# Kernel optimization log

Measured on AMD Instinct MI355X. Metric: run time of the kernel, lower is better.

Reference implementation:

```python
import jax, jax.numpy as jnp
import numpy as np

B, N, D, E, H = 4, 1024, 1024, 8, 4096


def setup_inputs() -> dict:
    key = jax.random.key(0)
    ks = jax.random.split(key, 8)
    x = jax.random.normal(ks[0], (B, N, D), dtype=jnp.float32)
    # gumbel noise, matching F.gumbel_softmax's -log(-log(U))
    u = jax.random.uniform(ks[1], (B * N, E), dtype=jnp.float32, minval=1e-9, maxval=1.0)
    gumbel = -jnp.log(-jnp.log(u))
    router_w = jax.random.normal(ks[2], (D, E), dtype=jnp.float32) * 0.02
    router_b = jnp.zeros((E,), dtype=jnp.float32)
    w1 = jax.random.normal(ks[3], (E, D, H), dtype=jnp.float32) * 0.02
    b1 = jnp.zeros((E, H), dtype=jnp.float32)
    w2 = jax.random.normal(ks[4], (E, H, D), dtype=jnp.float32) * 0.02
    b2 = jnp.zeros((E, D), dtype=jnp.float32)
    return {"x": x, "gumbel": gumbel, "router_w": router_w, "router_b": router_b,
            "w1": w1, "b1": b1, "w2": w2, "b2": b2}


def reference(x, gumbel, router_w, router_b, w1, b1, w2, b2):
    b, n, d = x.shape
    e = router_w.shape[1]
    xf = x.reshape(-1, d)                      # (T, D), T = B*N tokens
    logits = xf @ router_w + router_b          # (T, E)

    # hard gumbel-softmax with straight-through estimator (tau = 1.0)
    y_soft = jax.nn.softmax(logits + gumbel, axis=-1)
    hard = jax.nn.one_hot(jnp.argmax(y_soft, axis=-1), e, dtype=y_soft.dtype)
    weights = hard - jax.lax.stop_gradient(y_soft) + y_soft   # (T, E)

    # load-balancing aux loss
    probs = jax.nn.softmax(logits, axis=-1)
    count = jnp.maximum(jnp.float32(xf.shape[0]), 1.0)
    importance = probs.sum(axis=0) / count
    aux_loss = jnp.mean((importance - 1.0 / e) ** 2)

    # dense all-expert FFN: every expert processes every token
    hidden = jax.nn.gelu(jnp.einsum('td,edh->eth', xf, w1) + b1[:, None, :],
                         approximate=False)                    # (E, T, H)
    expert_out = jnp.einsum('eth,ehd->etd', hidden, w2) + b2[:, None, :]  # (E, T, D)

    # weighted combine (einsum 'ej,ejd->jd' in the original)
    out = jnp.einsum('te,etd->td', weights, expert_out)        # (T, D)
    return out.reshape(b, n, d), aux_loss
```

## Files before the change

kernel.cpp:

```cpp
#include <hip/hip_runtime.h>
#include <math.h>

#define D_DIM 1024
#define MAX_TILES 40

typedef __attribute__((ext_vector_type(4))) float f32x4;
typedef __attribute__((ext_vector_type(8))) short s16x8;

__device__ __forceinline__ unsigned short f2bf(float f){
  union { float f; unsigned u; } v; v.f = f;
  unsigned r = v.u + 0x7FFFu + ((v.u >> 16) & 1u);
  return (unsigned short)(r >> 16);
}

__device__ __forceinline__ void gld_lds16(const unsigned short* g, unsigned short* l){
  __builtin_amdgcn_global_load_lds(
      (const __attribute__((address_space(1))) unsigned int*)g,
      (__attribute__((address_space(3))) unsigned int*)l, 16, 0, 0);
}

template<int N>
__device__ __forceinline__ void wait_vmcnt(){
  if constexpr (N == 8)      asm volatile("s_waitcnt vmcnt(8)" ::: "memory");
  else if constexpr (N == 6) asm volatile("s_waitcnt vmcnt(6)" ::: "memory");
  else                       asm volatile("s_waitcnt vmcnt(0)" ::: "memory");
  __builtin_amdgcn_sched_barrier(0);
}

__global__ __launch_bounds__(256) void router_kernel(
    const float* __restrict__ x, const float* __restrict__ gumbel,
    const float* __restrict__ rw, const float* __restrict__ rb,
    int* __restrict__ expert_id, float* __restrict__ wtok,
    double* __restrict__ prob_sums, int* __restrict__ counts)
{
  int wave = threadIdx.x >> 6, lane = threadIdx.x & 63;
  int t = blockIdx.x * 4 + wave;
  const float* xr = x + (size_t)t * D_DIM;
  double acc[8];
  #pragma unroll
  for (int e = 0; e < 8; e++) acc[e] = 0.0;
  #pragma unroll
  for (int i = 0; i < 16; i++){
    int d = i * 64 + lane;
    double xv = (double)xr[d];
    const float4* rwp = (const float4*)(rw + (size_t)d * 8);
    float4 r0 = rwp[0], r1 = rwp[1];
    acc[0] += xv * (double)r0.x; acc[1] += xv * (double)r0.y;
    acc[2] += xv * (double)r0.z; acc[3] += xv * (double)r0.w;
    acc[4] += xv * (double)r1.x; acc[5] += xv * (double)r1.y;
    acc[6] += xv * (double)r1.z; acc[7] += xv * (double)r1.w;
  }
  #pragma unroll
  for (int e = 0; e < 8; e++){
    #pragma unroll
    for (int off = 32; off; off >>= 1) acc[e] += __shfl_xor(acc[e], off);
  }
  double logit[8], z[8];
  #pragma unroll
  for (int e = 0; e < 8; e++){
    logit[e] = acc[e] + (double)rb[e];
    z[e] = logit[e] + (double)gumbel[(size_t)t * 8 + e];
  }
  int amax = 0;
  #pragma unroll
  for (int e = 1; e < 8; e++) if (z[e] > z[amax]) amax = e;
  float zm = (float)z[amax];
  float se = 0.f;
  #pragma unroll
  for (int e = 0; e < 8; e++) se += expf((float)z[e] - zm);
  float y = 1.f / se;
  float w = (1.0f - y) + y;
  double lm = logit[0];
  #pragma unroll
  for (int e = 1; e < 8; e++) lm = fmax(lm, logit[e]);
  float p[8]; float ps = 0.f;
  #pragma unroll
  for (int e = 0; e < 8; e++){ p[e] = expf((float)(logit[e] - lm)); ps += p[e]; }
  float inv = 1.f / ps;

  __shared__ float sprob[4][8];
  if (lane == 0){
    expert_id[t] = amax; wtok[t] = w;
    atomicAdd(&counts[amax], 1);
    #pragma unroll
    for (int e = 0; e < 8; e++) sprob[wave][e] = p[e] * inv;
  }
  __syncthreads();
  if (threadIdx.x < 8){
    double s = (double)sprob[0][threadIdx.x] + (double)sprob[1][threadIdx.x]
             + (double)sprob[2][threadIdx.x] + (double)sprob[3][threadIdx.x];
    atomicAdd(&prob_sums[threadIdx.x], s);
  }
}

__global__ void finalize_kernel(const double* __restrict__ prob_sums, const int* __restrict__ counts,
                                int* __restrict__ offsets, int* __restrict__ cursor,
                                int* __restrict__ tile_e, int* __restrict__ tile_start,
                                int* __restrict__ tile_rows, int* __restrict__ n_mtiles,
                                float* __restrict__ aux_out)
{
  if (threadIdx.x == 0){
    int off = 0, m = 0;
    for (int e = 0; e < 8; e++){
      offsets[e] = off; cursor[e] = off;
      int c = counts[e];
      for (int by = 0; by * 128 < c; by++){
        tile_e[m] = e;
        tile_start[m] = off + by * 128;
        int r = c - by * 128;
        tile_rows[m] = r < 128 ? r : 128;
        m++;
      }
      off += c;
    }
    n_mtiles[0] = m;
    double aux = 0.0;
    for (int e = 0; e < 8; e++){
      double d = prob_sums[e] / 4096.0 - 0.125;
      aux += d * d;
    }
    aux_out[0] = (float)(aux / 8.0);
  }
}

__global__ __launch_bounds__(256) void scatter_kernel(
    const float* __restrict__ x, const int* __restrict__ expert_id, const float* __restrict__ wtok,
    int* __restrict__ cursor, int* __restrict__ token_of, float* __restrict__ gw,
    unsigned short* __restrict__ Xg)
{
  int t = blockIdx.x;
  __shared__ int spos;
  if (threadIdx.x == 0){
    int e = expert_id[t];
    int p = atomicAdd(&cursor[e], 1);
    spos = p;
    token_of[p] = t; gw[p] = wtok[t];
  }
  __syncthreads();
  int pos = spos;
  float4 v = ((const float4*)(x + (size_t)t * D_DIM))[threadIdx.x];
  ushort4 o; o.x = f2bf(v.x); o.y = f2bf(v.y); o.z = f2bf(v.z); o.w = f2bf(v.w);
  ((ushort4*)(Xg + (size_t)pos * D_DIM))[threadIdx.x] = o;
}

__global__ __launch_bounds__(256) void transpose_w(
    const float* __restrict__ W, unsigned short* __restrict__ WT, int K, int N)
{
  int e = blockIdx.z;
  int k0 = blockIdx.x * 64;
  int n0 = blockIdx.y * 64;
  __shared__ float tile[64][65];
  const float* src = W + (size_t)e * K * N;
  int tid = threadIdx.x;
  int r = tid >> 4;
  int c4 = (tid & 15) * 4;
  #pragma unroll
  for (int j = 0; j < 4; j++){
    int k = r + j * 16;
    float4 v = *(const float4*)(src + (size_t)(k0 + k) * N + n0 + c4);
    tile[k][c4] = v.x; tile[k][c4 + 1] = v.y; tile[k][c4 + 2] = v.z; tile[k][c4 + 3] = v.w;
  }
  __syncthreads();
  unsigned short* dst = WT + (size_t)e * N * K;
  #pragma unroll
  for (int it = 0; it < 2; it++){
    int idx = it * 256 + tid;
    int n = idx >> 3;
    int s = idx & 7;
    unsigned short buf[8];
    #pragma unroll
    for (int j = 0; j < 8; j++) buf[j] = f2bf(tile[s * 8 + j][n]);
    *(s16x8*)(dst + (size_t)(n0 + n) * K + k0 + s * 8) = *(s16x8*)buf;
  }
}

template<int K, int N, int BN, int PASS2>
__global__ __launch_bounds__(256, 2) void ffn_gemm(
    const unsigned short* __restrict__ A,
    const unsigned short* __restrict__ BT,
    const float* __restrict__ bias,
    const int* __restrict__ tile_e, const int* __restrict__ tile_start,
    const int* __restrict__ tile_rows, const int* __restrict__ n_mtiles,
    const int* __restrict__ token_of, const float* __restrict__ gw,
    unsigned short* __restrict__ Hout,
    float* __restrict__ Fout)
{
  int mt = blockIdx.y;
  if (mt >= n_mtiles[0]) return;
  int e = tile_e[mt], tstart = tile_start[mt], trows = tile_rows[mt];
  int bx = blockIdx.x;
  int tid = threadIdx.x, lane = tid & 63;
  int wv = __builtin_amdgcn_readfirstlane(tid >> 6);
  int wm = wv & 1, wn = wv >> 1;
  constexpr int NI    = BN / 32;
  constexpr int NBW   = BN / 32;
  constexpr int NK    = K / 64;
  constexpr int LOADS = 4 + NBW;

  __shared__ unsigned short sA[2][128 * 64];
  __shared__ unsigned short sB[2][BN * 64];

  int r8  = lane >> 3;
  int swz = ((lane & 7) ^ r8) * 8;

  const unsigned short* ap[4]; int al[4];
  #pragma unroll
  for (int j = 0; j < 4; j++){
    int c = wv * 4 + j;
    int row = c * 8 + r8;
    int rr = row < trows ? row : 0;
    ap[j] = A + (size_t)(tstart + rr) * K + swz;
    al[j] = c * 512;
  }
  const unsigned short* bp[NBW]; int bl[NBW];
  #pragma unroll
  for (int j = 0; j < NBW; j++){
    int c = wv * NBW + j;
    int n = bx * BN + c * 8 + r8;
    bp[j] = BT + ((size_t)e * N + n) * K + swz;
    bl[j] = c * 512;
  }

  f32x4 accv[4][NI];
  #pragma unroll
  for (int mi = 0; mi < 4; mi++)
    #pragma unroll
    for (int ni = 0; ni < NI; ni++) accv[mi][ni] = (f32x4){0.f, 0.f, 0.f, 0.f};

  #pragma unroll
  for (int b = 0; b < 2; b++){
    #pragma unroll
    for (int j = 0; j < 4; j++){ gld_lds16(ap[j], &sA[b][al[j]]); ap[j] += 64; }
    #pragma unroll
    for (int j = 0; j < NBW; j++){ gld_lds16(bp[j], &sB[b][bl[j]]); bp[j] += 64; }
  }

  int col = lane & 15, quad = lane >> 4, rx = col & 7;
  for (int kt = 0; kt < NK; ++kt){
    int cur = kt & 1;
    if (kt + 1 < NK) wait_vmcnt<LOADS>(); else wait_vmcnt<0>();
    __builtin_amdgcn_s_barrier();
    s16x8 af[2][4], bfr[2][NI];
    #pragma unroll
    for (int kh = 0; kh < 2; kh++){
      int ps = ((kh * 4 + quad) ^ rx) * 8;
      #pragma unroll
      for (int mi = 0; mi < 4; mi++)
        af[kh][mi] = *(const s16x8*)&sA[cur][(wm * 64 + mi * 16 + col) * 64 + ps];
      #pragma unroll
      for (int ni = 0; ni < NI; ni++)
        bfr[kh][ni] = *(const s16x8*)&sB[cur][(wn * (BN / 2) + ni * 16 + col) * 64 + ps];
    }
    asm volatile("s_waitcnt lgkmcnt(0)" ::: "memory");
    __builtin_amdgcn_sched_barrier(0);
    __builtin_amdgcn_s_barrier();
    if (kt + 2 < NK){
      #pragma unroll
      for (int j = 0; j < 4; j++){ gld_lds16(ap[j], &sA[cur][al[j]]); ap[j] += 64; }
      #pragma unroll
      for (int j = 0; j < NBW; j++){ gld_lds16(bp[j], &sB[cur][bl[j]]); bp[j] += 64; }
    }
    __builtin_amdgcn_s_setprio(1);
    #pragma unroll
    for (int kh = 0; kh < 2; kh++)
      #pragma unroll
      for (int mi = 0; mi < 4; mi++)
        #pragma unroll
        for (int ni = 0; ni < NI; ni++)
          accv[mi][ni] = __builtin_amdgcn_mfma_f32_16x16x32_bf16(af[kh][mi], bfr[kh][ni], accv[mi][ni], 0, 0, 0);
    __builtin_amdgcn_s_setprio(0);
  }

  float bv[NI];
  #pragma unroll
  for (int ni = 0; ni < NI; ni++)
    bv[ni] = bias[(size_t)e * N + bx * BN + wn * (BN / 2) + ni * 16 + col];

  if (PASS2 == 0){
    #pragma unroll
    for (int mi = 0; mi < 4; mi++){
      int rbase = wm * 64 + mi * 16 + quad * 4;
      #pragma unroll
      for (int r = 0; r < 4; r++){
        int row = rbase + r;
        if (row < trows){
          size_t orow = (size_t)(tstart + row) * N + bx * BN + wn * (BN / 2) + col;
          #pragma unroll
          for (int ni = 0; ni < NI; ni++){
            float v = accv[mi][ni][r] + bv[ni];
            float g = 0.5f * v * (1.0f + erff(v * 0.70710678118654752f));
            Hout[orow + ni * 16] = f2bf(g);
          }
        }
      }
    }
  } else {
    #pragma unroll
    for (int mi = 0; mi < 4; mi++){
      int rbase = wm * 64 + mi * 16 + quad * 4;
      #pragma unroll
      for (int r = 0; r < 4; r++){
        int row = rbase + r;
        if (row < trows){
          int pos = tstart + row;
          int tok = token_of[pos];
          float wgt = gw[pos];
          size_t orow = (size_t)tok * N + bx * BN + wn * (BN / 2) + col;
          #pragma unroll
          for (int ni = 0; ni < NI; ni++)
            Fout[orow + ni * 16] = (accv[mi][ni][r] + bv[ni]) * wgt;
        }
      }
    }
  }
}

extern "C" void kernel_launch(void* const* d_in, const int* in_sizes, int n_in,
                              void* d_out, int out_size, void* d_ws, size_t ws_size,
                              hipStream_t stream)
{
  const float* x      = (const float*)d_in[0];
  const float* gumbel = (const float*)d_in[1];
  const float* rw     = (const float*)d_in[2];
  const float* rb     = (const float*)d_in[3];
  const float* w1     = (const float*)d_in[4];
  const float* b1     = (const float*)d_in[5];
  const float* w2     = (const float*)d_in[6];
  const float* b2     = (const float*)d_in[7];
  float* out = (float*)d_out;

  char* ws = (char*)d_ws;
  double* prob_sums = (double*)(ws + 0);
  int* counts     = (int*)(ws + 64);
  int* offsets    = (int*)(ws + 96);
  int* cursor     = (int*)(ws + 128);
  int* n_mtiles   = (int*)(ws + 160);
  int* tile_e     = (int*)(ws + 192);
  int* tile_start = (int*)(ws + 384);
  int* tile_rows  = (int*)(ws + 576);
  int* expert_id  = (int*)(ws + 1024);
  float* wtok     = (float*)(ws + 1024 + 16384);
  int* token_of   = (int*)(ws + 1024 + 2 * 16384);
  float* gw       = (float*)(ws + 1024 + 3 * 16384);
  unsigned short* Xg     = (unsigned short*)(ws + 66560);
  unsigned short* hidden = (unsigned short*)(ws + 66560 + 8388608);
  unsigned short* wT     = (unsigned short*)(ws + 66560 + 8388608 + 33554432);

  hipMemsetAsync(ws, 0, 256, stream);

  router_kernel<<<1024, 256, 0, stream>>>(x, gumbel, rw, rb, expert_id, wtok, prob_sums, counts);
  finalize_kernel<<<1, 64, 0, stream>>>(prob_sums, counts, offsets, cursor,
                                        tile_e, tile_start, tile_rows, n_mtiles, out + 4194304);
  scatter_kernel<<<4096, 256, 0, stream>>>(x, expert_id, wtok, cursor, token_of, gw, Xg);

  transpose_w<<<dim3(16, 64, 8), 256, 0, stream>>>(w1, wT, 1024, 4096);
  ffn_gemm<1024, 4096, 128, 0><<<dim3(32, MAX_TILES), 256, 0, stream>>>(
      Xg, wT, b1, tile_e, tile_start, tile_rows, n_mtiles, nullptr, nullptr, hidden, nullptr);

  transpose_w<<<dim3(64, 16, 8), 256, 0, stream>>>(w2, wT, 4096, 1024);
  ffn_gemm<4096, 1024, 64, 1><<<dim3(16, MAX_TILES), 256, 0, stream>>>(
      hidden, wT, b2, tile_e, tile_start, tile_rows, n_mtiles, token_of, gw, nullptr, out);
}
```

Before: 544.8 us.

## Fuse weight transposes with router and scatter, widen second GEMM tile

Merges the w1 transpose with the router kernel and the w2 transpose with the token scatter kernel, so each pair runs as one launch with heterogeneous blocks. The two transposed weights now get separate workspace buffers, which allows the merge. The GEMM is fixed at a 128-wide N tile for both passes, so the second GEMM uses half as many blocks. Its k-loop is also restructured to issue the MFMAs for the first k-half while the second half's LDS reads are still in flight. This removes launch gaps and some serialization, at the cost of more workspace and less parallelism in the second GEMM.

```diff
diff --git a/kernel.cpp b/kernel.cpp
--- a/kernel.cpp
+++ b/kernel.cpp
@@ -19,22 +19,15 @@
       (__attribute__((address_space(3))) unsigned int*)l, 16, 0, 0);
 }
 
-template<int N>
-__device__ __forceinline__ void wait_vmcnt(){
-  if constexpr (N == 8)      asm volatile("s_waitcnt vmcnt(8)" ::: "memory");
-  else if constexpr (N == 6) asm volatile("s_waitcnt vmcnt(6)" ::: "memory");
-  else                       asm volatile("s_waitcnt vmcnt(0)" ::: "memory");
-  __builtin_amdgcn_sched_barrier(0);
-}
-
-__global__ __launch_bounds__(256) void router_kernel(
+__device__ __forceinline__ void router_body(
     const float* __restrict__ x, const float* __restrict__ gumbel,
     const float* __restrict__ rw, const float* __restrict__ rb,
     int* __restrict__ expert_id, float* __restrict__ wtok,
-    double* __restrict__ prob_sums, int* __restrict__ counts)
+    double* __restrict__ prob_sums, int* __restrict__ counts,
+    int rb_idx, float* sprob )
 {
   int wave = threadIdx.x >> 6, lane = threadIdx.x & 63;
-  int t = blockIdx.x * 4 + wave;
+  int t = rb_idx * 4 + wave;
   const float* xr = x + (size_t)t * D_DIM;
   double acc[8];
   #pragma unroll
@@ -78,18 +71,64 @@
   for (int e = 0; e < 8; e++){ p[e] = expf((float)(logit[e] - lm)); ps += p[e]; }
   float inv = 1.f / ps;
 
-  __shared__ float sprob[4][8];
   if (lane == 0){
     expert_id[t] = amax; wtok[t] = w;
     atomicAdd(&counts[amax], 1);
     #pragma unroll
-    for (int e = 0; e < 8; e++) sprob[wave][e] = p[e] * inv;
+    for (int e = 0; e < 8; e++) sprob[wave * 8 + e] = p[e] * inv;
   }
   __syncthreads();
   if (threadIdx.x < 8){
-    double s = (double)sprob[0][threadIdx.x] + (double)sprob[1][threadIdx.x]
-             + (double)sprob[2][threadIdx.x] + (double)sprob[3][threadIdx.x];
+    double s = (double)sprob[0 * 8 + threadIdx.x] + (double)sprob[1 * 8 + threadIdx.x]
+             + (double)sprob[2 * 8 + threadIdx.x] + (double)sprob[3 * 8 + threadIdx.x];
     atomicAdd(&prob_sums[threadIdx.x], s);
+  }
+}
+
+__device__ __forceinline__ void transpose_body(
+    const float* __restrict__ W, unsigned short* __restrict__ WT,
+    int K, int N, int kx, int ny, int e, float* tile )
+{
+  int k0 = kx * 64;
+  int n0 = ny * 64;
+  const float* src = W + (size_t)e * K * N;
+  int tid = threadIdx.x;
+  int r = tid >> 4;
+  int c4 = (tid & 15) * 4;
+  #pragma unroll
+  for (int j = 0; j < 4; j++){
+    int k = r + j * 16;
+    float4 v = *(const float4*)(src + (size_t)(k0 + k) * N + n0 + c4);
+    tile[k * 65 + c4] = v.x; tile[k * 65 + c4 + 1] = v.y;
+    tile[k * 65 + c4 + 2] = v.z; tile[k * 65 + c4 + 3] = v.w;
+  }
+  __syncthreads();
+  unsigned short* dst = WT + (size_t)e * N * K;
+  #pragma unroll
+  for (int it = 0; it < 2; it++){
+    int idx = it * 256 + tid;
+    int n = idx >> 3;
+    int s = idx & 7;
+    unsigned short buf[8];
+    #pragma unroll
+    for (int j = 0; j < 8; j++) buf[j] = f2bf(tile[(s * 8 + j) * 65 + n]);
+    *(s16x8*)(dst + (size_t)(n0 + n) * K + k0 + s * 8) = *(s16x8*)buf;
+  }
+}
+
+__global__ __launch_bounds__(256) void stage_a(
+    const float* __restrict__ w1, unsigned short* __restrict__ wT1,
+    const float* __restrict__ x, const float* __restrict__ gumbel,
+    const float* __restrict__ rw, const float* __restrict__ rb,
+    int* __restrict__ expert_id, float* __restrict__ wtok,
+    double* __restrict__ prob_sums, int* __restrict__ counts)
+{
+  __shared__ float smem[64 * 65];
+  int b = blockIdx.x;
+  if (b < 8192){
+    transpose_body(w1, wT1, 1024, 4096, b & 15, (b >> 4) & 63, b >> 10, smem);
+  } else {
+    router_body(x, gumbel, rw, rb, expert_id, wtok, prob_sums, counts, b - 8192, smem);
   }
 }
 
@@ -123,58 +162,35 @@
   }
 }
 
-__global__ __launch_bounds__(256) void scatter_kernel(
-    const float* __restrict__ x, const int* __restrict__ expert_id, const float* __restrict__ wtok,
-    int* __restrict__ cursor, int* __restrict__ token_of, float* __restrict__ gw,
+__global__ __launch_bounds__(256) void stage_b(
+    const float* __restrict__ w2, unsigned short* __restrict__ wT2,
+    const float* __restrict__ x, const int* __restrict__ expert_id,
+    const float* __restrict__ wtok, int* __restrict__ cursor,
+    int* __restrict__ token_of, float* __restrict__ gw,
     unsigned short* __restrict__ Xg)
 {
-  int t = blockIdx.x;
-  __shared__ int spos;
-  if (threadIdx.x == 0){
-    int e = expert_id[t];
-    int p = atomicAdd(&cursor[e], 1);
-    spos = p;
-    token_of[p] = t; gw[p] = wtok[t];
-  }
-  __syncthreads();
-  int pos = spos;
-  float4 v = ((const float4*)(x + (size_t)t * D_DIM))[threadIdx.x];
-  ushort4 o; o.x = f2bf(v.x); o.y = f2bf(v.y); o.z = f2bf(v.z); o.w = f2bf(v.w);
-  ((ushort4*)(Xg + (size_t)pos * D_DIM))[threadIdx.x] = o;
-}
-
-__global__ __launch_bounds__(256) void transpose_w(
-    const float* __restrict__ W, unsigned short* __restrict__ WT, int K, int N)
-{
-  int e = blockIdx.z;
-  int k0 = blockIdx.x * 64;
-  int n0 = blockIdx.y * 64;
-  __shared__ float tile[64][65];
-  const float* src = W + (size_t)e * K * N;
-  int tid = threadIdx.x;
-  int r = tid >> 4;
-  int c4 = (tid & 15) * 4;
-  #pragma unroll
-  for (int j = 0; j < 4; j++){
-    int k = r + j * 16;
-    float4 v = *(const float4*)(src + (size_t)(k0 + k) * N + n0 + c4);
-    tile[k][c4] = v.x; tile[k][c4 + 1] = v.y; tile[k][c4 + 2] = v.z; tile[k][c4 + 3] = v.w;
-  }
-  __syncthreads();
-  unsigned short* dst = WT + (size_t)e * N * K;
-  #pragma unroll
-  for (int it = 0; it < 2; it++){
-    int idx = it * 256 + tid;
-    int n = idx >> 3;
-    int s = idx & 7;
-    unsigned short buf[8];
-    #pragma unroll
-    for (int j = 0; j < 8; j++) buf[j] = f2bf(tile[s * 8 + j][n]);
-    *(s16x8*)(dst + (size_t)(n0 + n) * K + k0 + s * 8) = *(s16x8*)buf;
-  }
-}
-
-template<int K, int N, int BN, int PASS2>
+  __shared__ float smem[64 * 65];
+  int b = blockIdx.x;
+  if (b < 8192){
+    transpose_body(w2, wT2, 4096, 1024, b & 63, (b >> 6) & 15, b >> 10, smem);
+  } else {
+    int t = b - 8192;
+    int* spos = (int*)smem;
+    if (threadIdx.x == 0){
+      int e = expert_id[t];
+      int p = atomicAdd(&cursor[e], 1);
+      spos[0] = p;
+      token_of[p] = t; gw[p] = wtok[t];
+    }
+    __syncthreads();
+    int pos = spos[0];
+    float4 v = ((const float4*)(x + (size_t)t * D_DIM))[threadIdx.x];
+    ushort4 o; o.x = f2bf(v.x); o.y = f2bf(v.y); o.z = f2bf(v.z); o.w = f2bf(v.w);
+    ((ushort4*)(Xg + (size_t)pos * D_DIM))[threadIdx.x] = o;
+  }
+}
+
+template<int K, int N, int PASS2>
 __global__ __launch_bounds__(256, 2) void ffn_gemm(
     const unsigned short* __restrict__ A,
     const unsigned short* __restrict__ BT,
@@ -192,13 +208,10 @@
   int tid = threadIdx.x, lane = tid & 63;
   int wv = __builtin_amdgcn_readfirstlane(tid >> 6);
   int wm = wv & 1, wn = wv >> 1;
-  constexpr int NI    = BN / 32;
-  constexpr int NBW   = BN / 32;
-  constexpr int NK    = K / 64;
-  constexpr int LOADS = 4 + NBW;
+  constexpr int NK = K / 64;
 
   __shared__ unsigned short sA[2][128 * 64];
-  __shared__ unsigned short sB[2][BN * 64];
+  __shared__ unsigned short sB[2][128 * 64];
 
   int r8  = lane >> 3;
   int swz = ((lane & 7) ^ r8) * 8;
@@ -212,45 +225,60 @@
     ap[j] = A + (size_t)(tstart + rr) * K + swz;
     al[j] = c * 512;
   }
-  const unsigned short* bp[NBW]; int bl[NBW];
-  #pragma unroll
-  for (int j = 0; j < NBW; j++){
-    int c = wv * NBW + j;
-    int n = bx * BN + c * 8 + r8;
+  const unsigned short* bp[4]; int bl[4];
+  #pragma unroll
+  for (int j = 0; j < 4; j++){
+    int c = wv * 4 + j;
+    int n = bx * 128 + c * 8 + r8;
     bp[j] = BT + ((size_t)e * N + n) * K + swz;
     bl[j] = c * 512;
   }
 
-  f32x4 accv[4][NI];
+  f32x4 accv[4][4];
   #pragma unroll
   for (int mi = 0; mi < 4; mi++)
     #pragma unroll
-    for (int ni = 0; ni < NI; ni++) accv[mi][ni] = (f32x4){0.f, 0.f, 0.f, 0.f};
+    for (int ni = 0; ni < 4; ni++) accv[mi][ni] = (f32x4){0.f, 0.f, 0.f, 0.f};
 
   #pragma unroll
   for (int b = 0; b < 2; b++){
     #pragma unroll
     for (int j = 0; j < 4; j++){ gld_lds16(ap[j], &sA[b][al[j]]); ap[j] += 64; }
     #pragma unroll
-    for (int j = 0; j < NBW; j++){ gld_lds16(bp[j], &sB[b][bl[j]]); bp[j] += 64; }
+    for (int j = 0; j < 4; j++){ gld_lds16(bp[j], &sB[b][bl[j]]); bp[j] += 64; }
   }
 
   int col = lane & 15, quad = lane >> 4, rx = col & 7;
+  int ps0 = (quad ^ rx) * 8;
+  int ps1 = ((4 + quad) ^ rx) * 8;
   for (int kt = 0; kt < NK; ++kt){
     int cur = kt & 1;
-    if (kt + 1 < NK) wait_vmcnt<LOADS>(); else wait_vmcnt<0>();
+    if (kt + 1 < NK) asm volatile("s_waitcnt vmcnt(8)" ::: "memory");
+    else             asm volatile("s_waitcnt vmcnt(0)" ::: "memory");
+    __builtin_amdgcn_sched_barrier(0);
     __builtin_amdgcn_s_barrier();
-    s16x8 af[2][4], bfr[2][NI];
-    #pragma unroll
-    for (int kh = 0; kh < 2; kh++){
-      int ps = ((kh * 4 + quad) ^ rx) * 8;
-      #pragma unroll
-      for (int mi = 0; mi < 4; mi++)
-        af[kh][mi] = *(const s16x8*)&sA[cur][(wm * 64 + mi * 16 + col) * 64 + ps];
-      #pragma unroll
-      for (int ni = 0; ni < NI; ni++)
-        bfr[kh][ni] = *(const s16x8*)&sB[cur][(wn * (BN / 2) + ni * 16 + col) * 64 + ps];
-    }
+    s16x8 af0[4], bf0[4], af1[4], bf1[4];
+    #pragma unroll
+    for (int mi = 0; mi < 4; mi++)
+      af0[mi] = *(const s16x8*)&sA[cur][(wm * 64 + mi * 16 + col) * 64 + ps0];
+    #pragma unroll
+    for (int ni = 0; ni < 4; ni++)
+      bf0[ni] = *(const s16x8*)&sB[cur][(wn * 64 + ni * 16 + col) * 64 + ps0];
+    #pragma unroll
+    for (int mi = 0; mi < 4; mi++)
+      af1[mi] = *(const s16x8*)&sA[cur][(wm * 64 + mi * 16 + col) * 64 + ps1];
+    #pragma unroll
+    for (int ni = 0; ni < 4; ni++)
+      bf1[ni] = *(const s16x8*)&sB[cur][(wn * 64 + ni * 16 + col) * 64 + ps1];
+    asm volatile("s_waitcnt lgkmcnt(8)" ::: "memory");
+    __builtin_amdgcn_sched_barrier(0);
+    __builtin_amdgcn_s_setprio(1);
+    #pragma unroll
+    for (int mi = 0; mi < 4; mi++)
+      #pragma unroll
+      for (int ni = 0; ni < 4; ni++)
+        accv[mi][ni] = __builtin_amdgcn_mfma_f32_16x16x32_bf16(af0[mi], bf0[ni], accv[mi][ni], 0, 0, 0);
+    __builtin_amdgcn_s_setprio(0);
     asm volatile("s_waitcnt lgkmcnt(0)" ::: "memory");
     __builtin_amdgcn_sched_barrier(0);
     __builtin_amdgcn_s_barrier();
@@ -258,23 +286,21 @@
       #pragma unroll
       for (int j = 0; j < 4; j++){ gld_lds16(ap[j], &sA[cur][al[j]]); ap[j] += 64; }
       #pragma unroll
-      for (int j = 0; j < NBW; j++){ gld_lds16(bp[j], &sB[cur][bl[j]]); bp[j] += 64; }
+      for (int j = 0; j < 4; j++){ gld_lds16(bp[j], &sB[cur][bl[j]]); bp[j] += 64; }
     }
     __builtin_amdgcn_s_setprio(1);
     #pragma unroll
-    for (int kh = 0; kh < 2; kh++)
-      #pragma unroll
-      for (int mi = 0; mi < 4; mi++)
-        #pragma unroll
-        for (int ni = 0; ni < NI; ni++)
-          accv[mi][ni] = __builtin_amdgcn_mfma_f32_16x16x32_bf16(af[kh][mi], bfr[kh][ni], accv[mi][ni], 0, 0, 0);
+    for (int mi = 0; mi < 4; mi++)
+      #pragma unroll
+      for (int ni = 0; ni < 4; ni++)
+        accv[mi][ni] = __builtin_amdgcn_mfma_f32_16x16x32_bf16(af1[mi], bf1[ni], accv[mi][ni], 0, 0, 0);
     __builtin_amdgcn_s_setprio(0);
   }
 
-  float bv[NI];
-  #pragma unroll
-  for (int ni = 0; ni < NI; ni++)
-    bv[ni] = bias[(size_t)e * N + bx * BN + wn * (BN / 2) + ni * 16 + col];
+  float bv[4];
+  #pragma unroll
+  for (int ni = 0; ni < 4; ni++)
+    bv[ni] = bias[(size_t)e * N + bx * 128 + wn * 64 + ni * 16 + col];
 
   if (PASS2 == 0){
     #pragma unroll
@@ -284,9 +310,9 @@
       for (int r = 0; r < 4; r++){
         int row = rbase + r;
         if (row < trows){
-          size_t orow = (size_t)(tstart + row) * N + bx * BN + wn * (BN / 2) + col;
+          size_t orow = (size_t)(tstart + row) * N + bx * 128 + wn * 64 + col;
           #pragma unroll
-          for (int ni = 0; ni < NI; ni++){
+          for (int ni = 0; ni < 4; ni++){
             float v = accv[mi][ni][r] + bv[ni];
             float g = 0.5f * v * (1.0f + erff(v * 0.70710678118654752f));
             Hout[orow + ni * 16] = f2bf(g);
@@ -305,9 +331,9 @@
           int pos = tstart + row;
           int tok = token_of[pos];
           float wgt = gw[pos];
-          size_t orow = (size_t)tok * N + bx * BN + wn * (BN / 2) + col;
+          size_t orow = (size_t)tok * N + bx * 128 + wn * 64 + col;
           #pragma unroll
-          for (int ni = 0; ni < NI; ni++)
+          for (int ni = 0; ni < 4; ni++)
             Fout[orow + ni * 16] = (accv[mi][ni][r] + bv[ni]) * wgt;
         }
       }
@@ -344,20 +370,21 @@
   float* gw       = (float*)(ws + 1024 + 3 * 16384);
   unsigned short* Xg     = (unsigned short*)(ws + 66560);
   unsigned short* hidden = (unsigned short*)(ws + 66560 + 8388608);
-  unsigned short* wT     = (unsigned short*)(ws + 66560 + 8388608 + 33554432);
+  unsigned short* wT1    = (unsigned short*)(ws + 66560 + 8388608 + 33554432);
+  unsigned short* wT2    = (unsigned short*)(ws + 66560 + 8388608 + 33554432 + 67108864);
 
   hipMemsetAsync(ws, 0, 256, stream);
 
-  router_kernel<<<1024, 256, 0, stream>>>(x, gumbel, rw, rb, expert_id, wtok, prob_sums, counts);
+  stage_a<<<8192 + 1024, 256, 0, stream>>>(w1, wT1, x, gumbel, rw, rb,
+                                           expert_id, wtok, prob_sums, counts);
   finalize_kernel<<<1, 64, 0, stream>>>(prob_sums, counts, offsets, cursor,
                                         tile_e, tile_start, tile_rows, n_mtiles, out + 4194304);
-  scatter_kernel<<<4096, 256, 0, stream>>>(x, expert_id, wtok, cursor, token_of, gw, Xg);
-
-  transpose_w<<<dim3(16, 64, 8), 256, 0, stream>>>(w1, wT, 1024, 4096);
-  ffn_gemm<1024, 4096, 128, 0><<<dim3(32, MAX_TILES), 256, 0, stream>>>(
-      Xg, wT, b1, tile_e, tile_start, tile_rows, n_mtiles, nullptr, nullptr, hidden, nullptr);
-
-  transpose_w<<<dim3(64, 16, 8), 256, 0, stream>>>(w2, wT, 4096, 1024);
-  ffn_gemm<4096, 1024, 64, 1><<<dim3(16, MAX_TILES), 256, 0, stream>>>(
-      hidden, wT, b2, tile_e, tile_start, tile_rows, n_mtiles, token_of, gw, nullptr, out);
-}
+  stage_b<<<8192 + 4096, 256, 0, stream>>>(w2, wT2, x, expert_id, wtok, cursor,
+                                           token_of, gw, Xg);
+
+  ffn_gemm<1024, 4096, 0><<<dim3(32, MAX_TILES), 256, 0, stream>>>(
+      Xg, wT1, b1, tile_e, tile_start, tile_rows, n_mtiles, nullptr, nullptr, hidden, nullptr);
+
+  ffn_gemm<4096, 1024, 1><<<dim3(8, MAX_TILES), 256, 0, stream>>>(
+      hidden, wT2, b2, tile_e, tile_start, tile_rows, n_mtiles, token_of, gw, nullptr, out);
+}
```

New measurement: 566.8 us. +4.0%, slower.
